# Performance work log

Hardware: AMD Instinct MI355X
Metric: run time of the kernel (lower is better)

The kernel has to match this reference:

```python
import jax, jax.numpy as jnp
import numpy as np

H = 8
DH = 64  # dim_head = dim // h
SCALE = DH ** -0.5
MEM_LEN = 512
CMEM_LEN = 128
RATIO = 4
SEQ_LEN = 512


def setup_inputs() -> dict:
    key = jax.random.key(0)
    ks = jax.random.split(key, 10)
    b, t, d = 8, 512, 512
    s = 0.02
    return {
        'x': jax.random.normal(ks[0], (b, t, d), jnp.float32),
        'mem': jax.random.normal(ks[1], (b, MEM_LEN, d), jnp.float32),
        'cmem': jax.random.normal(ks[2], (b, CMEM_LEN, d), jnp.float32),
        'Wq': jax.random.normal(ks[3], (d, d), jnp.float32) * s,
        'Wkv': jax.random.normal(ks[4], (2 * d, d), jnp.float32) * s,
        'Wo': jax.random.normal(ks[5], (d, d), jnp.float32) * s,
        'bo': jnp.zeros((d,), jnp.float32),
        'conv_w': jax.random.normal(ks[6], (d, d, RATIO), jnp.float32) * s,  # Conv1d OIH
        'conv_b': jnp.zeros((d,), jnp.float32),
        'deconv_w': jax.random.normal(ks[7], (MEM_LEN, CMEM_LEN), jnp.float32) * s,  # Linear(cmem_len, mem_len)
        'deconv_b': jnp.zeros((MEM_LEN,), jnp.float32),
    }


def _merge_heads(t):
    b, n, _ = t.shape
    return t.reshape(b, n, H, DH).transpose(0, 2, 1, 3)  # [b,h,n,dh]


def _full_attn(q, k, v):
    dots = jnp.einsum('bhid,bhjd->bhij', q, k) * (q.shape[-1] ** -0.5)
    return jnp.einsum('bhij,bhjd->bhid', jax.nn.softmax(dots, axis=-1), v)


def reference(x, mem, cmem, Wq, Wkv, Wo, bo, conv_w, conv_b, deconv_w, deconv_b):
    b, t, d = x.shape
    mem_len, cmem_len = mem.shape[1], cmem.shape[1]
    # projections
    q = x @ Wq.T
    kv_input = jnp.concatenate([cmem, mem, x], axis=1)  # [b, kv_len, d]
    kv = kv_input @ Wkv.T
    k, v = jnp.split(kv, 2, axis=-1)
    q, k, v = map(_merge_heads, (q, k, v))
    # main attention with causal mask offset by total memory length
    dots = jnp.einsum('bhid,bhjd->bhij', q, k) * SCALE  # [b,h,t,kv_len]
    total_mem = mem_len + cmem_len
    neg = -jnp.finfo(dots.dtype).max
    i = jnp.arange(t)[:, None]
    j = jnp.arange(t + total_mem)[None, :]
    causal = j > (i + total_mem)  # triu(diagonal=1+total_mem)
    dots = jnp.where(causal[None, None], neg, dots)
    attn = jax.nn.softmax(dots, axis=-1)
    out = jnp.einsum('bhij,bhjd->bhid', attn, v).transpose(0, 2, 1, 3).reshape(b, t, d)
    logits = out @ Wo.T + bo
    # FIFO memory update
    queue = jnp.concatenate([mem, x], axis=1)
    old_mem = jax.lax.stop_gradient(queue[:, :queue.shape[1] - MEM_LEN])  # evicted, detached
    new_mem = queue[:, -MEM_LEN:]
    # conv compression (old_mem length == SEQ_LEN, divisible by RATIO -> no pad)
    cm = jax.lax.conv_general_dilated(old_mem.transpose(0, 2, 1), conv_w, (RATIO,), 'VALID',
                                      dimension_numbers=('NCH', 'OIH', 'NCH'))
    compressed = (cm + conv_b[None, :, None]).transpose(0, 2, 1)  # [b, L/ratio, d]
    new_cmem = jnp.concatenate([cmem, compressed], axis=1)[:, -CMEM_LEN:]
    # reconstruction attention loss
    ckv = compressed @ Wkv.T
    cmem_k, cmem_v = map(_merge_heads, jnp.split(ckv, 2, axis=-1))
    kv_len = k.shape[2]
    lo = kv_len - min(mem_len, MEM_LEN) - SEQ_LEN
    hi = kv_len - SEQ_LEN
    qd = jax.lax.stop_gradient(q)
    omk = jax.lax.stop_gradient(k[:, :, lo:hi])
    omv = jax.lax.stop_gradient(v[:, :, lo:hi])
    aux_loss = jnp.mean((_full_attn(qd, omk, omv) - _full_attn(qd, cmem_k, cmem_v)) ** 2)
    # autoencoding loss via deconv Linear(cmem_len -> mem_len) over the seq axis
    recon = (new_cmem.transpose(0, 2, 1) @ deconv_w.T + deconv_b).transpose(0, 2, 1)  # [b, MEM_LEN, d]
    ae_loss = jnp.mean((old_mem - recon) ** 2)
    return (logits, new_mem, new_cmem, aux_loss, ae_loss)
```

## Files before the change

kernel.cpp:

```cpp
#include <hip/hip_runtime.h>

typedef __bf16 bf16x8 __attribute__((ext_vector_type(8)));
typedef float f32x4 __attribute__((ext_vector_type(4)));
typedef float f32x16 __attribute__((ext_vector_type(16)));
typedef unsigned short u16;
typedef unsigned int u32;

#define TLEN 512
#define DMODEL 512
#define DH 64
#define KVLEN 1152
#define TOTALMEM 640

__device__ inline u16 f2b(float f) {
    union { float f; u32 u; } x; x.f = f;
    u32 u = x.u;
    return (u16)((u + 0x7FFFu + ((u >> 16) & 1u)) >> 16);
}

__device__ inline float wave_red_sum(float v) {
#pragma unroll
    for (int off = 1; off < 64; off <<= 1) v += __shfl_xor(v, off);
    return v;
}

__device__ inline void gload16(const u16* g, u16* l) {
    __builtin_amdgcn_global_load_lds((const __attribute__((address_space(1))) void*)g,
                                     (__attribute__((address_space(3))) void*)l, 16, 0, 0);
}

__device__ __forceinline__ u32 cvtpk_bf16(float lo, float hi) {
    u32 r;
    asm("v_cvt_pk_bf16_f32 %0, %1, %2" : "=v"(r) : "v"(lo), "v"(hi));
    return r;
}

__global__ __launch_bounds__(256)
void prep_kernel(const float* __restrict__ x, const float* __restrict__ mem,
                 const float* __restrict__ cmem, const float* __restrict__ Wq,
                 const float* __restrict__ Wkv, const float* __restrict__ Wo,
                 const float* __restrict__ cw, const float* __restrict__ dw,
                 u16* __restrict__ kvin, u16* __restrict__ wq_b, u16* __restrict__ wkv_b,
                 u16* __restrict__ wo_b, u16* __restrict__ cw2, u16* __restrict__ dwb,
                 float* __restrict__ newmem, float* __restrict__ accs) {
    int idx = blockIdx.x * 256 + threadIdx.x;
    if (idx == 0) { accs[0] = 0.f; accs[1] = 0.f; accs[2] = 0.f; accs[3] = 0.f; }
    int e = idx * 4;
    float4 v;
    u16* o;
    if (e < 4718592) {
        int row = e >> 9, col = e & 511;
        int b = row / KVLEN, p = row - b * KVLEN;
        const float* src;
        if (p < 128)       src = cmem + ((size_t)(b * 128 + p)) * 512 + col;
        else if (p < 640)  src = mem  + ((size_t)(b * 512 + (p - 128))) * 512 + col;
        else               src = x    + ((size_t)(b * 512 + (p - 640))) * 512 + col;
        v = *(const float4*)src;
        o = kvin + e;
        if (p >= 640)
            *(float4*)(newmem + ((size_t)(b * 512 + (p - 640)) * 512 + col)) = v;
    } else if (e < 4980736) {
        int t = e - 4718592; v = *(const float4*)(Wq + t); o = wq_b + t;
    } else if (e < 5505024) {
        int t = e - 4980736; v = *(const float4*)(Wkv + t); o = wkv_b + t;
    } else if (e < 5767168) {
        int t = e - 5505024; v = *(const float4*)(Wo + t); o = wo_b + t;
    } else if (e < 6815744) {
        int t = e - 5767168;
        int oo = t >> 11, rem = t & 2047, tt = rem >> 9, ii = rem & 511;
        const float* s0 = cw + oo * 2048 + tt;
        v.x = s0[(ii + 0) * 4]; v.y = s0[(ii + 1) * 4];
        v.z = s0[(ii + 2) * 4]; v.w = s0[(ii + 3) * 4];
        o = cw2 + t;
    } else {
        int t = e - 6815744;
        v = *(const float4*)(dw + t); o = dwb + t;
    }
    o[0] = f2b(v.x); o[1] = f2b(v.y); o[2] = f2b(v.z); o[3] = f2b(v.w);
}

__device__ __forceinline__ void gemm_dev(
    const u16* __restrict__ A, int lda, int rowsPerB, long long bstride,
    const u16* __restrict__ Bt, int ldb, int Kb,
    float* __restrict__ Cpart, int partStride,
    float* __restrict__ Cf, u16* __restrict__ Cb, int ldc,
    const float* __restrict__ bias,
    int bx, int by, int bz, u16* As, u16* Bs) {
    const int tid = threadIdx.x;
    const int lane = tid & 63, wave = tid >> 6;
    const int wr = (wave >> 1) * 64, wc = (wave & 1) * 64;
    const int fr = lane & 15, fg = lane >> 4;
    const int arow0 = bx * 128;
    const int brow0 = by * 128;
    const int k0start = bz * Kb;

    const int lrow = lane >> 2;
    const int lcol = (lane & 3) * 8;
    const u16* gA[2]; const u16* gB[2];
#pragma unroll
    for (int i = 0; i < 2; ++i) {
        int r = wave * 32 + i * 16 + lrow;
        int gr = arow0 + r;
        int bb = gr / rowsPerB;
        int lr = gr - bb * rowsPerB;
        gA[i] = A + (size_t)bb * bstride + (size_t)lr * lda + k0start + lcol;
        gB[i] = Bt + (size_t)(brow0 + r) * ldb + k0start + lcol;
    }
    u16* lA0 = &As[(wave * 32) * 32];
    u16* lA1 = &As[(wave * 32 + 16) * 32];
    u16* lB0 = &Bs[(wave * 32) * 32];
    u16* lB1 = &Bs[(wave * 32 + 16) * 32];

    f32x4 acc[4][4] = {};
    for (int k = 0; k < Kb; k += 32) {
        __syncthreads();
        gload16(gA[0] + k, lA0);
        gload16(gA[1] + k, lA1);
        gload16(gB[0] + k, lB0);
        gload16(gB[1] + k, lB1);
        __syncthreads();
        bf16x8 af[4], bfr[4];
#pragma unroll
        for (int m = 0; m < 4; ++m) af[m] = *(bf16x8*)&As[(wr + m * 16 + fr) * 32 + fg * 8];
#pragma unroll
        for (int n = 0; n < 4; ++n) bfr[n] = *(bf16x8*)&Bs[(wc + n * 16 + fr) * 32 + fg * 8];
#pragma unroll
        for (int m = 0; m < 4; ++m)
#pragma unroll
            for (int n = 0; n < 4; ++n)
                acc[m][n] = __builtin_amdgcn_mfma_f32_16x16x32_bf16(af[m], bfr[n], acc[m][n], 0, 0, 0);
    }

#pragma unroll
    for (int m = 0; m < 4; ++m)
#pragma unroll
        for (int n = 0; n < 4; ++n)
#pragma unroll
            for (int r = 0; r < 4; ++r) {
                int row = arow0 + wr + m * 16 + fg * 4 + r;
                int col = brow0 + wc + n * 16 + fr;
                float v = acc[m][n][r];
                if (Cpart) {
                    Cpart[(size_t)bz * partStride + (size_t)row * ldc + col] = v;
                } else {
                    if (bias) v += bias[col];
                    if (Cf) Cf[(size_t)row * ldc + col] = v;
                    if (Cb) Cb[(size_t)row * ldc + col] = f2b(v);
                }
            }
}

__global__ __launch_bounds__(256)
void gemm3(const u16* __restrict__ kvin, const u16* __restrict__ wq,
           const u16* __restrict__ wkv, const u16* __restrict__ cw2,
           u16* __restrict__ q_bf, u16* __restrict__ kv_bf, float* __restrict__ part) {
    __shared__ u16 As[128 * 32];
    __shared__ u16 Bs[128 * 32];
    int id = blockIdx.x;
    if (id < 128) {
        gemm_dev(kvin + 327680, 512, 512, 589824, wq, 512, 512,
                 nullptr, 0, nullptr, q_bf, 512, nullptr,
                 id & 31, id >> 5, 0, As, Bs);
    } else if (id < 704) {
        int t = id - 128;
        gemm_dev(kvin, 512, 9216, 0, wkv, 512, 512,
                 nullptr, 0, nullptr, kv_bf, 1024, nullptr,
                 t % 72, t / 72, 0, As, Bs);
    } else {
        int t = id - 704;
        gemm_dev(kvin + 65536, 2048, 128, 589824, cw2, 2048, 512,
                 part, 524288, nullptr, nullptr, 512, nullptr,
                 t & 7, (t >> 3) & 3, t >> 5, As, Bs);
    }
}

__global__ __launch_bounds__(256)
void gemm_full(const u16* __restrict__ A, int lda, int rowsPerB, long long bstride,
               const u16* __restrict__ Bt, int ldb, int Kb,
               float* __restrict__ Cf, u16* __restrict__ Cb, int ldc,
               const float* __restrict__ bias) {
    __shared__ u16 As[128 * 32];
    __shared__ u16 Bs[128 * 32];
    gemm_dev(A, lda, rowsPerB, bstride, Bt, ldb, Kb, nullptr, 0, Cf, Cb, ldc,
             bias, blockIdx.x, blockIdx.y, 0, As, Bs);
}

__global__ __launch_bounds__(256)
void conv_reduce(const float* __restrict__ part, const float* __restrict__ cb,
                 float* __restrict__ outf, u16* __restrict__ outb) {
    int idx = (blockIdx.x * 256 + threadIdx.x) * 4;
    float4 s = *(const float4*)(part + idx);
#pragma unroll
    for (int sp = 1; sp < 4; ++sp) {
        float4 p = *(const float4*)(part + (size_t)sp * 524288 + idx);
        s.x += p.x; s.y += p.y; s.z += p.z; s.w += p.w;
    }
    float4 bb = *(const float4*)(cb + (idx & 511));
    s.x += bb.x; s.y += bb.y; s.z += bb.z; s.w += bb.w;
    *(float4*)(outf + idx) = s;
    outb[idx + 0] = f2b(s.x); outb[idx + 1] = f2b(s.y);
    outb[idx + 2] = f2b(s.z); outb[idx + 3] = f2b(s.w);
}

__device__ __forceinline__ void transpose_dev(const u16* __restrict__ kv,
                                              u16* __restrict__ vT, int rowsPerB,
                                              int jt, int bh, u16* t_s) {
    int b = bh >> 3, h = bh & 7;
    int tid = threadIdx.x;
    int jr = tid >> 2, c0 = (tid & 3) * 16;
    const u16* g = kv + (size_t)(b * rowsPerB + jt * 64 + jr) * 1024 + 512 + h * DH + c0;
#pragma unroll
    for (int u = 0; u < 16; ++u) t_s[jr * 65 + c0 + u] = g[u];
    __syncthreads();
    int dh = tid >> 2, j0 = (tid & 3) * 16;
    union { u16 us[8]; bf16x8 v8; } o1, o2;
#pragma unroll
    for (int u = 0; u < 8; ++u) {
        o1.us[u] = t_s[(j0 + u) * 65 + dh];
        o2.us[u] = t_s[(j0 + 8 + u) * 65 + dh];
    }
    u16* o = vT + (size_t)(bh * DH + dh) * rowsPerB + jt * 64 + j0;
    *(bf16x8*)o = o1.v8;
    *(bf16x8*)(o + 8) = o2.v8;
}

__global__ __launch_bounds__(256)
void transpose2(const u16* __restrict__ kv, u16* __restrict__ vTm_,
                const u16* __restrict__ ckv, u16* __restrict__ vTc_,
                const u16* __restrict__ comp, u16* __restrict__ compT) {
    __shared__ u16 t_s[64 * 65];
    int bx = blockIdx.x, bh = blockIdx.y;
    if (bx < 18) { transpose_dev(kv, vTm_, KVLEN, bx, bh, t_s); return; }
    if (bx < 20) { transpose_dev(ckv, vTc_, 128, bx - 18, bh, t_s); return; }
    int idq = (bx - 20) * 64 + bh;
    int b = idq >> 4, tile = idq & 15;
    int rt = tile >> 3, ct = tile & 7;
    int tid = threadIdx.x;
    int jr = tid >> 2, c0 = (tid & 3) * 16;
    const u16* g = comp + (size_t)(b * 128 + rt * 64 + jr) * 512 + ct * 64 + c0;
#pragma unroll
    for (int u = 0; u < 16; ++u) t_s[jr * 65 + c0 + u] = g[u];
    __syncthreads();
    int dh = tid >> 2, j0 = (tid & 3) * 16;
    union { u16 us[8]; bf16x8 v8; } o1, o2;
#pragma unroll
    for (int u = 0; u < 8; ++u) {
        o1.us[u] = t_s[(j0 + u) * 65 + dh];
        o2.us[u] = t_s[(j0 + 8 + u) * 65 + dh];
    }
    u16* o = compT + (size_t)(b * 512 + ct * 64 + dh) * 128 + rt * 64 + j0;
    *(bf16x8*)o = o1.v8;
    *(bf16x8*)(o + 8) = o2.v8;
}

template <bool MASK>
__device__ __forceinline__ void attn_pass(
    const u16* __restrict__ kbase, int kstride,
    const u16* __restrict__ vbase, int vstride,
    int njt, int tid, int iq_min,
    const bf16x8* qf, u16* k_s, u16* v_s,
    f32x16& o0, f32x16& o1, float& m_run, float& l_run)
{
    const int lane = tid & 63;
    const int c31 = lane & 31;
    const int hi = lane >> 5;
    const int hi4 = hi << 2;
    const int srow = tid >> 2, ssl = tid & 3;
    const int kwa = srow * 64 + ((ssl ^ (srow & 7)) << 3);
    const int kwb = srow * 64 + (((ssl + 4) ^ (srow & 7)) << 3);
    const int iq = iq_min + c31;

    int krd[2][4];
#pragma unroll
    for (int jsub = 0; jsub < 2; ++jsub) {
        int row = jsub * 32 + c31;
#pragma unroll
        for (int ks = 0; ks < 4; ++ks)
            krd[jsub][ks] = row * 64 + (((2 * ks + hi) ^ (row & 7)) << 3);
    }
    int vrd[2][4];
#pragma unroll
    for (int half = 0; half < 2; ++half) {
        int row = half * 32 + c31;
#pragma unroll
        for (int s = 0; s < 4; ++s)
            vrd[half][s] = row * 64 + (((2 * s + hi) ^ (row & 7)) << 3);
    }

    float4 lk0, lk1, lv0, lv1;
#define AT_LOAD(T) { \
        const u16* gk = kbase + (size_t)((T) * 64 + srow) * kstride + ssl * 8; \
        lk0 = *(const float4*)gk; lk1 = *(const float4*)(gk + 32); \
        const u16* gv = vbase + (size_t)srow * vstride + (T) * 64 + ssl * 8; \
        lv0 = *(const float4*)gv; lv1 = *(const float4*)(gv + 32); }
#define AT_STORE(B) { \
        u16* kd = k_s + (B) * 4096; u16* vd = v_s + (B) * 4096; \
        *(float4*)(kd + kwa) = lk0; *(float4*)(kd + kwb) = lk1; \
        *(float4*)(vd + kwa) = lv0; *(float4*)(vd + kwb) = lv1; }

    AT_LOAD(0); AT_STORE(0);
    __syncthreads();

    for (int t = 0; t < njt; ++t) {
        const int cur = t & 1;
        if (t + 1 < njt) AT_LOAD(t + 1);
        const u16* ks_ = k_s + cur * 4096;
        const u16* vs_ = v_s + cur * 4096;

        f32x16 sA = {}, sB = {};
#pragma unroll
        for (int ks = 0; ks < 4; ++ks) {
            bf16x8 a0 = *(const bf16x8*)&ks_[krd[0][ks]];
            sA = __builtin_amdgcn_mfma_f32_32x32x16_bf16(a0, qf[ks], sA, 0, 0, 0);
        }
#pragma unroll
        for (int ks = 0; ks < 4; ++ks) {
            bf16x8 a1 = *(const bf16x8*)&ks_[krd[1][ks]];
            sB = __builtin_amdgcn_mfma_f32_32x32x16_bf16(a1, qf[ks], sB, 0, 0, 0);
        }
        if (MASK) {
            if (t * 64 + 63 > iq_min + TOTALMEM) {
#pragma unroll
                for (int r = 0; r < 16; ++r) {
                    int rj = (r & 3) + 8 * (r >> 2) + hi4;
                    if (t * 64 + rj > iq + TOTALMEM) sA[r] = -1e30f;
                    if (t * 64 + 32 + rj > iq + TOTALMEM) sB[r] = -1e30f;
                }
            }
        }
        float tmax = sA[0];
#pragma unroll
        for (int r = 1; r < 16; ++r) tmax = fmaxf(tmax, sA[r]);
#pragma unroll
        for (int r = 0; r < 16; ++r) tmax = fmaxf(tmax, sB[r]);
        tmax = fmaxf(tmax, __shfl_xor(tmax, 32));
        tmax *= 0.125f;
        if (__any(tmax > m_run + 8.0f)) {
            float m_new = fmaxf(m_run, tmax);
            float scl = __expf(m_run - m_new);
            m_run = m_new;
            l_run *= scl;
#pragma unroll
            for (int r = 0; r < 16; ++r) {
                float sc = __shfl(scl, (r & 3) + 8 * (r >> 2) + hi4);
                o0[r] *= sc; o1[r] *= sc;
            }
        }
        const float negm = -m_run;
        float ps = 0.f;
#pragma unroll
        for (int jsub = 0; jsub < 2; ++jsub) {
#pragma unroll
            for (int ksub = 0; ksub < 2; ++ksub) {
                float p0 = __expf(fmaf((jsub ? sB[ksub * 8 + 0] : sA[ksub * 8 + 0]), 0.125f, negm));
                float p1 = __expf(fmaf((jsub ? sB[ksub * 8 + 1] : sA[ksub * 8 + 1]), 0.125f, negm));
                float p2 = __expf(fmaf((jsub ? sB[ksub * 8 + 2] : sA[ksub * 8 + 2]), 0.125f, negm));
                float p3 = __expf(fmaf((jsub ? sB[ksub * 8 + 3] : sA[ksub * 8 + 3]), 0.125f, negm));
                float p4 = __expf(fmaf((jsub ? sB[ksub * 8 + 4] : sA[ksub * 8 + 4]), 0.125f, negm));
                float p5 = __expf(fmaf((jsub ? sB[ksub * 8 + 5] : sA[ksub * 8 + 5]), 0.125f, negm));
                float p6 = __expf(fmaf((jsub ? sB[ksub * 8 + 6] : sA[ksub * 8 + 6]), 0.125f, negm));
                float p7 = __expf(fmaf((jsub ? sB[ksub * 8 + 7] : sA[ksub * 8 + 7]), 0.125f, negm));
                ps += ((p0 + p1) + (p2 + p3)) + ((p4 + p5) + (p6 + p7));
                u32 X = cvtpk_bf16(p0, p1);
                u32 Z = cvtpk_bf16(p2, p3);
                u32 Y = cvtpk_bf16(p4, p5);
                u32 W = cvtpk_bf16(p6, p7);
                auto s1 = __builtin_amdgcn_permlane32_swap(X, Y, false, false);
                auto s2 = __builtin_amdgcn_permlane32_swap(Z, W, false, false);
                union { u32 w[4]; bf16x8 v; } fa;
                fa.w[0] = (u32)s1[0]; fa.w[1] = (u32)s2[0];
                fa.w[2] = (u32)s1[1]; fa.w[3] = (u32)s2[1];
                bf16x8 bv0 = *(const bf16x8*)&vs_[vrd[0][jsub * 2 + ksub]];
                bf16x8 bv1 = *(const bf16x8*)&vs_[vrd[1][jsub * 2 + ksub]];
                o0 = __builtin_amdgcn_mfma_f32_32x32x16_bf16(fa.v, bv0, o0, 0, 0, 0);
                o1 = __builtin_amdgcn_mfma_f32_32x32x16_bf16(fa.v, bv1, o1, 0, 0, 0);
            }
        }
        ps += __shfl_xor(ps, 32);
        l_run += ps;
        if (t + 1 < njt) AT_STORE(cur ^ 1);
        __syncthreads();
    }
#undef AT_LOAD
#undef AT_STORE
}

__global__ __launch_bounds__(256)
void attn_fused(const u16* __restrict__ q_bf, const u16* __restrict__ kv,
                const u16* __restrict__ vTm_, const u16* __restrict__ ckv,
                const u16* __restrict__ vTc_, u16* __restrict__ out_bf,
                float* __restrict__ acc_sum) {
    __shared__ u16 k_s[2 * 4096];
    __shared__ u16 v_s[2 * 4096];
    __shared__ float red_s[4];
    const int id = blockIdx.x;
    const int tid = threadIdx.x;
    const int w = tid >> 6, lane = tid & 63;
    const int c31 = lane & 31, hi4 = (lane >> 5) << 2;

    if (id < 256) {
        const int it = id & 3, bh = id >> 2;
        const int b = bh >> 3, h = bh & 7;
        const int iwmin = it * 128 + w * 32;
        const int iq = iwmin + c31;

        bf16x8 qf[4];
#pragma unroll
        for (int ks = 0; ks < 4; ++ks)
            qf[ks] = *(const bf16x8*)&q_bf[(size_t)(b * TLEN + iq) * DMODEL + h * DH + ks * 16 + hi4 * 2];

        const u16* kbase = kv + (size_t)b * KVLEN * 1024 + h * DH;
        const u16* vbase = vTm_ + (size_t)(bh * DH) * KVLEN;
        const int njt = ((it * 128 + 767) >> 6) + 1;

        f32x16 o0 = {}, o1 = {};
        float m_run = -1e30f, l_run = 0.f;
        attn_pass<true>(kbase, 1024, vbase, KVLEN, njt, tid, iwmin, qf, k_s, v_s, o0, o1, m_run, l_run);

        float linv = 1.0f / l_run;
#pragma unroll
        for (int r = 0; r < 16; ++r) {
            int R = (r & 3) + 8 * (r >> 2) + hi4;
            float li = __shfl(linv, R);
            int i = iwmin + R;
            u16* o = out_bf + (size_t)(b * TLEN + i) * DMODEL + h * DH + c31;
            o[0]  = f2b(o0[r] * li);
            o[32] = f2b(o1[r] * li);
        }
    } else {
        const int t2 = id - 256;
        const int it = t2 & 3, bh = t2 >> 2;
        const int b = bh >> 3, h = bh & 7;
        const int iwmin = it * 128 + w * 32;
        const int iq = iwmin + c31;

        bf16x8 qf[4];
#pragma unroll
        for (int ks = 0; ks < 4; ++ks)
            qf[ks] = *(const bf16x8*)&q_bf[(size_t)(b * TLEN + iq) * DMODEL + h * DH + ks * 16 + hi4 * 2];

        f32x16 o0 = {}, o1 = {};
        float m_run = -1e30f, l_run = 0.f;
        attn_pass<false>(kv + (size_t)(b * KVLEN + 128) * 1024 + h * DH, 1024,
                         vTm_ + (size_t)(bh * DH) * KVLEN + 128, KVLEN, 8,
                         tid, 0, qf, k_s, v_s, o0, o1, m_run, l_run);
        float n0[16], n1[16];
        {
            float linv = 1.0f / l_run;
#pragma unroll
            for (int r = 0; r < 16; ++r) {
                float li = __shfl(linv, (r & 3) + 8 * (r >> 2) + hi4);
                n0[r] = o0[r] * li;
                n1[r] = o1[r] * li;
            }
        }
        f32x16 c0 = {}, c1 = {};
        m_run = -1e30f; l_run = 0.f;
        attn_pass<false>(ckv + (size_t)(b * 128) * 1024 + h * DH, 1024,
                         vTc_ + (size_t)(bh * DH) * 128, 128, 2,
                         tid, 0, qf, k_s, v_s, c0, c1, m_run, l_run);
        float lsum = 0.f;
        {
            float linv = 1.0f / l_run;
#pragma unroll
            for (int r = 0; r < 16; ++r) {
                float li = __shfl(linv, (r & 3) + 8 * (r >> 2) + hi4);
                float d0 = n0[r] - c0[r] * li;
                float d1 = n1[r] - c1[r] * li;
                lsum += d0 * d0 + d1 * d1;
            }
        }
        lsum = wave_red_sum(lsum);
        if (lane == 0) red_s[w] = lsum;
        __syncthreads();
        if (tid == 0) atomicAdd(acc_sum, red_s[0] + red_s[1] + red_s[2] + red_s[3]);
    }
}

__global__ __launch_bounds__(256)
void tail2(const u16* __restrict__ attn_bf, const u16* __restrict__ wo_b,
           const float* __restrict__ bo, float* __restrict__ logits,
           const u16* __restrict__ dwb, const u16* __restrict__ compT,
           const float* __restrict__ mem, const float* __restrict__ db,
           float* __restrict__ accs, float* __restrict__ scal_out) {
    __shared__ __align__(16) char smem[16400];
    const int id = blockIdx.x;
    const int tid = threadIdx.x;
    u16* As = (u16*)smem;
    u16* Bs = (u16*)(smem + 8192);

    if (id < 128) {
        gemm_dev(attn_bf, 512, 4096, 0, wo_b, 512, 512,
                 nullptr, 0, logits, nullptr, 512, bo, id & 31, id >> 5, 0, As, Bs);
        return;
    }
    float* red = (float*)(smem + 16384);
    const int t = id - 128;
    const int b = t >> 4;
    const int bx = (t >> 2) & 3, by = t & 3;
    const int lane = tid & 63, wave = tid >> 6;
    const int wr = (wave >> 1) * 64, wc = (wave & 1) * 64;
    const int fr = lane & 15, fg = lane >> 4;
    const int arow0 = bx * 128, brow0 = by * 128;
    const int lrow = lane >> 2, lcol = (lane & 3) * 8;
    const u16* gA[2]; const u16* gB[2];
#pragma unroll
    for (int i = 0; i < 2; ++i) {
        int r = wave * 32 + i * 16 + lrow;
        gA[i] = dwb + (size_t)(arow0 + r) * 128 + lcol;
        gB[i] = compT + (size_t)(b * 512 + brow0 + r) * 128 + lcol;
    }
    u16* lA0 = &As[(wave * 32) * 32];
    u16* lA1 = &As[(wave * 32 + 16) * 32];
    u16* lB0 = &Bs[(wave * 32) * 32];
    u16* lB1 = &Bs[(wave * 32 + 16) * 32];

    f32x4 acc[4][4] = {};
    for (int k = 0; k < 128; k += 32) {
        __syncthreads();
        gload16(gA[0] + k, lA0);
        gload16(gA[1] + k, lA1);
        gload16(gB[0] + k, lB0);
        gload16(gB[1] + k, lB1);
        __syncthreads();
        bf16x8 af[4], bfr[4];
#pragma unroll
        for (int m = 0; m < 4; ++m) af[m] = *(bf16x8*)&As[(wr + m * 16 + fr) * 32 + fg * 8];
#pragma unroll
        for (int n = 0; n < 4; ++n) bfr[n] = *(bf16x8*)&Bs[(wc + n * 16 + fr) * 32 + fg * 8];
#pragma unroll
        for (int m = 0; m < 4; ++m)
#pragma unroll
            for (int n = 0; n < 4; ++n)
                acc[m][n] = __builtin_amdgcn_mfma_f32_16x16x32_bf16(af[m], bfr[n], acc[m][n], 0, 0, 0);
    }

    float lsum = 0.f;
#pragma unroll
    for (int m = 0; m < 4; ++m)
#pragma unroll
        for (int n = 0; n < 4; ++n)
#pragma unroll
            for (int rr = 0; rr < 4; ++rr) {
                int row = arow0 + wr + m * 16 + fg * 4 + rr;
                int col = brow0 + wc + n * 16 + fr;
                float v = acc[m][n][rr] + db[row];
                float d = mem[(size_t)(b * 512 + row) * 512 + col] - v;
                lsum = fmaf(d, d, lsum);
            }
    lsum = wave_red_sum(lsum);
    if (lane == 0) red[wave] = lsum;
    __syncthreads();
    if (tid == 0) {
        atomicAdd(accs + 1, red[0] + red[1] + red[2] + red[3]);
        __threadfence();
        u32 c = atomicAdd((u32*)(accs + 2), 1u);
        if (c == 127u) {
            float a0 = atomicAdd(accs + 0, 0.f);
            float a1 = atomicAdd(accs + 1, 0.f);
            scal_out[0] = a0 * (1.f / 2097152.f);
            scal_out[1] = a1 * (1.f / 2097152.f);
        }
    }
}

extern "C" void kernel_launch(void* const* d_in, const int* in_sizes, int n_in,
                              void* d_out, int out_size, void* d_ws, size_t ws_size,
                              hipStream_t stream) {
    const float* x      = (const float*)d_in[0];
    const float* mem    = (const float*)d_in[1];
    const float* cmem   = (const float*)d_in[2];
    const float* Wq     = (const float*)d_in[3];
    const float* Wkv    = (const float*)d_in[4];
    const float* Wo     = (const float*)d_in[5];
    const float* bo     = (const float*)d_in[6];
    const float* conv_w = (const float*)d_in[7];
    const float* conv_b = (const float*)d_in[8];
    const float* deconv_w = (const float*)d_in[9];
    const float* deconv_b = (const float*)d_in[10];
    float* out = (float*)d_out;

    char* w = (char*)d_ws;
    auto alloc = [&](size_t bytes) { char* p = w; w += (bytes + 255) & ~255ull; return p; };
    u16* Wq_bf   = (u16*)alloc(262144 * 2);
    u16* Wkv_bf  = (u16*)alloc(524288 * 2);
    u16* Wo_bf   = (u16*)alloc(262144 * 2);
    u16* cw2_bf  = (u16*)alloc(1048576 * 2);
    u16* dwb_bf  = (u16*)alloc(65536 * 2);
    u16* kvin_bf = (u16*)alloc(4718592 * 2);
    u16* q_bf    = (u16*)alloc(2097152 * 2);
    u16* kv_bf   = (u16*)alloc(9437184 * 2);
    u16* comp_bf = (u16*)alloc(524288 * 2);
    u16* compT   = (u16*)alloc(524288 * 2);
    u16* ckv_bf  = (u16*)alloc(1048576 * 2);
    u16* vTm     = (u16*)alloc(4718592 * 2);
    u16* vTc     = (u16*)alloc(524288 * 2);
    u16* attn_bf = (u16*)alloc(2097152 * 2);
    float* part  = (float*)alloc(4 * 524288 * 4);
    float* accs  = (float*)alloc(256);

    float* logits_o  = out;
    float* newmem_o  = out + 2097152;
    float* newcmem_o = out + 4194304;
    float* scalars_o = out + 4718592;

    prep_kernel<<<6720, 256, 0, stream>>>(x, mem, cmem, Wq, Wkv, Wo, conv_w, deconv_w,
                                          kvin_bf, Wq_bf, Wkv_bf, Wo_bf, cw2_bf, dwb_bf,
                                          newmem_o, accs);

    gemm3<<<832, 256, 0, stream>>>(kvin_bf, Wq_bf, Wkv_bf, cw2_bf, q_bf, kv_bf, part);

    conv_reduce<<<512, 256, 0, stream>>>(part, conv_b, newcmem_o, comp_bf);

    gemm_full<<<dim3(8, 8), 256, 0, stream>>>(comp_bf, 512, 1024, 0, Wkv_bf, 512, 512,
                                              nullptr, ckv_bf, 1024, nullptr);

    transpose2<<<dim3(22, 64), 256, 0, stream>>>(kv_bf, vTm, ckv_bf, vTc, comp_bf, compT);

    attn_fused<<<512, 256, 0, stream>>>(q_bf, kv_bf, vTm, ckv_bf, vTc, attn_bf, accs);

    tail2<<<256, 256, 0, stream>>>(attn_bf, Wo_bf, bo, logits_o,
                                   dwb_bf, compT, mem, deconv_b,
                                   accs, scalars_o);
}
```

Before: 126.2 us.

## Drop split-K conv GEMM and regroup mid-stage kernels to cut launches

The conv compression GEMM now runs with its full K=2048 in 32 blocks that write bias-added fp32 and bf16 outputs directly, so the partial-sum buffer and the conv_reduce kernel are gone. These long-K blocks are scheduled first in gemm3 so they start early. The compressed-KV GEMM, the comp transpose and the V transpose are merged into one mid kernel, with a small separate kernel for the cmem V transpose. Launch count drops by one and the partial-sum round-trip is removed, at the cost of a long serial K loop on only 32 blocks, which may become the critical path.

```diff
diff --git a/kernel.cpp b/kernel.cpp
--- a/kernel.cpp
+++ b/kernel.cpp
@@ -82,17 +82,15 @@
 __device__ __forceinline__ void gemm_dev(
     const u16* __restrict__ A, int lda, int rowsPerB, long long bstride,
     const u16* __restrict__ Bt, int ldb, int Kb,
-    float* __restrict__ Cpart, int partStride,
     float* __restrict__ Cf, u16* __restrict__ Cb, int ldc,
     const float* __restrict__ bias,
-    int bx, int by, int bz, u16* As, u16* Bs) {
+    int bx, int by, u16* As, u16* Bs) {
     const int tid = threadIdx.x;
     const int lane = tid & 63, wave = tid >> 6;
     const int wr = (wave >> 1) * 64, wc = (wave & 1) * 64;
     const int fr = lane & 15, fg = lane >> 4;
     const int arow0 = bx * 128;
     const int brow0 = by * 128;
-    const int k0start = bz * Kb;
 
     const int lrow = lane >> 2;
     const int lcol = (lane & 3) * 8;
@@ -103,8 +101,8 @@
         int gr = arow0 + r;
         int bb = gr / rowsPerB;
         int lr = gr - bb * rowsPerB;
-        gA[i] = A + (size_t)bb * bstride + (size_t)lr * lda + k0start + lcol;
-        gB[i] = Bt + (size_t)(brow0 + r) * ldb + k0start + lcol;
+        gA[i] = A + (size_t)bb * bstride + (size_t)lr * lda + lcol;
+        gB[i] = Bt + (size_t)(brow0 + r) * ldb + lcol;
     }
     u16* lA0 = &As[(wave * 32) * 32];
     u16* lA1 = &As[(wave * 32 + 16) * 32];
@@ -140,66 +138,33 @@
                 int row = arow0 + wr + m * 16 + fg * 4 + r;
                 int col = brow0 + wc + n * 16 + fr;
                 float v = acc[m][n][r];
-                if (Cpart) {
-                    Cpart[(size_t)bz * partStride + (size_t)row * ldc + col] = v;
-                } else {
-                    if (bias) v += bias[col];
-                    if (Cf) Cf[(size_t)row * ldc + col] = v;
-                    if (Cb) Cb[(size_t)row * ldc + col] = f2b(v);
-                }
+                if (bias) v += bias[col];
+                if (Cf) Cf[(size_t)row * ldc + col] = v;
+                if (Cb) Cb[(size_t)row * ldc + col] = f2b(v);
             }
 }
 
 __global__ __launch_bounds__(256)
 void gemm3(const u16* __restrict__ kvin, const u16* __restrict__ wq,
            const u16* __restrict__ wkv, const u16* __restrict__ cw2,
-           u16* __restrict__ q_bf, u16* __restrict__ kv_bf, float* __restrict__ part) {
+           const float* __restrict__ conv_b,
+           u16* __restrict__ q_bf, u16* __restrict__ kv_bf,
+           float* __restrict__ newcmem, u16* __restrict__ comp_bf) {
     __shared__ u16 As[128 * 32];
     __shared__ u16 Bs[128 * 32];
     int id = blockIdx.x;
-    if (id < 128) {
+    if (id < 32) {
+        gemm_dev(kvin + 65536, 2048, 128, 589824, cw2, 2048, 2048,
+                 newcmem, comp_bf, 512, conv_b, id & 7, id >> 3, As, Bs);
+    } else if (id < 160) {
+        int t = id - 32;
         gemm_dev(kvin + 327680, 512, 512, 589824, wq, 512, 512,
-                 nullptr, 0, nullptr, q_bf, 512, nullptr,
-                 id & 31, id >> 5, 0, As, Bs);
-    } else if (id < 704) {
-        int t = id - 128;
+                 nullptr, q_bf, 512, nullptr, t & 31, t >> 5, As, Bs);
+    } else {
+        int t = id - 160;
         gemm_dev(kvin, 512, 9216, 0, wkv, 512, 512,
-                 nullptr, 0, nullptr, kv_bf, 1024, nullptr,
-                 t % 72, t / 72, 0, As, Bs);
-    } else {
-        int t = id - 704;
-        gemm_dev(kvin + 65536, 2048, 128, 589824, cw2, 2048, 512,
-                 part, 524288, nullptr, nullptr, 512, nullptr,
-                 t & 7, (t >> 3) & 3, t >> 5, As, Bs);
-    }
-}
-
-__global__ __launch_bounds__(256)
-void gemm_full(const u16* __restrict__ A, int lda, int rowsPerB, long long bstride,
-               const u16* __restrict__ Bt, int ldb, int Kb,
-               float* __restrict__ Cf, u16* __restrict__ Cb, int ldc,
-               const float* __restrict__ bias) {
-    __shared__ u16 As[128 * 32];
-    __shared__ u16 Bs[128 * 32];
-    gemm_dev(A, lda, rowsPerB, bstride, Bt, ldb, Kb, nullptr, 0, Cf, Cb, ldc,
-             bias, blockIdx.x, blockIdx.y, 0, As, Bs);
-}
-
-__global__ __launch_bounds__(256)
-void conv_reduce(const float* __restrict__ part, const float* __restrict__ cb,
-                 float* __restrict__ outf, u16* __restrict__ outb) {
-    int idx = (blockIdx.x * 256 + threadIdx.x) * 4;
-    float4 s = *(const float4*)(part + idx);
-#pragma unroll
-    for (int sp = 1; sp < 4; ++sp) {
-        float4 p = *(const float4*)(part + (size_t)sp * 524288 + idx);
-        s.x += p.x; s.y += p.y; s.z += p.z; s.w += p.w;
-    }
-    float4 bb = *(const float4*)(cb + (idx & 511));
-    s.x += bb.x; s.y += bb.y; s.z += bb.z; s.w += bb.w;
-    *(float4*)(outf + idx) = s;
-    outb[idx + 0] = f2b(s.x); outb[idx + 1] = f2b(s.y);
-    outb[idx + 2] = f2b(s.z); outb[idx + 3] = f2b(s.w);
+                 nullptr, kv_bf, 1024, nullptr, t % 72, t / 72, As, Bs);
+    }
 }
 
 __device__ __forceinline__ void transpose_dev(const u16* __restrict__ kv,
@@ -225,32 +190,49 @@
 }
 
 __global__ __launch_bounds__(256)
-void transpose2(const u16* __restrict__ kv, u16* __restrict__ vTm_,
-                const u16* __restrict__ ckv, u16* __restrict__ vTc_,
-                const u16* __restrict__ comp, u16* __restrict__ compT) {
+void mid_kernel(const u16* __restrict__ comp, const u16* __restrict__ wkv,
+                u16* __restrict__ ckv, u16* __restrict__ compT,
+                const u16* __restrict__ kv, u16* __restrict__ vTm_) {
+    __shared__ __align__(16) char smem[16640];
+    int id = blockIdx.x;
+    int tid = threadIdx.x;
+    if (id < 64) {
+        u16* As = (u16*)smem;
+        u16* Bs = (u16*)(smem + 8192);
+        gemm_dev(comp, 512, 1024, 0, wkv, 512, 512,
+                 nullptr, ckv, 1024, nullptr, id & 7, id >> 3, As, Bs);
+        return;
+    }
+    u16* t_s = (u16*)smem;
+    if (id < 192) {
+        int idq = id - 64;
+        int b = idq >> 4, tile = idq & 15;
+        int rt = tile >> 3, ct = tile & 7;
+        int jr = tid >> 2, c0 = (tid & 3) * 16;
+        const u16* g = comp + (size_t)(b * 128 + rt * 64 + jr) * 512 + ct * 64 + c0;
+#pragma unroll
+        for (int u = 0; u < 16; ++u) t_s[jr * 65 + c0 + u] = g[u];
+        __syncthreads();
+        int dh = tid >> 2, j0 = (tid & 3) * 16;
+        union { u16 us[8]; bf16x8 v8; } o1, o2;
+#pragma unroll
+        for (int u = 0; u < 8; ++u) {
+            o1.us[u] = t_s[(j0 + u) * 65 + dh];
+            o2.us[u] = t_s[(j0 + 8 + u) * 65 + dh];
+        }
+        u16* o = compT + (size_t)(b * 512 + ct * 64 + dh) * 128 + rt * 64 + j0;
+        *(bf16x8*)o = o1.v8;
+        *(bf16x8*)(o + 8) = o2.v8;
+        return;
+    }
+    int t = id - 192;
+    transpose_dev(kv, vTm_, KVLEN, t % 18, t / 18, t_s);
+}
+
+__global__ __launch_bounds__(256)
+void vtc_kernel(const u16* __restrict__ ckv, u16* __restrict__ vTc_) {
     __shared__ u16 t_s[64 * 65];
-    int bx = blockIdx.x, bh = blockIdx.y;
-    if (bx < 18) { transpose_dev(kv, vTm_, KVLEN, bx, bh, t_s); return; }
-    if (bx < 20) { transpose_dev(ckv, vTc_, 128, bx - 18, bh, t_s); return; }
-    int idq = (bx - 20) * 64 + bh;
-    int b = idq >> 4, tile = idq & 15;
-    int rt = tile >> 3, ct = tile & 7;
-    int tid = threadIdx.x;
-    int jr = tid >> 2, c0 = (tid & 3) * 16;
-    const u16* g = comp + (size_t)(b * 128 + rt * 64 + jr) * 512 + ct * 64 + c0;
-#pragma unroll
-    for (int u = 0; u < 16; ++u) t_s[jr * 65 + c0 + u] = g[u];
-    __syncthreads();
-    int dh = tid >> 2, j0 = (tid & 3) * 16;
-    union { u16 us[8]; bf16x8 v8; } o1, o2;
-#pragma unroll
-    for (int u = 0; u < 8; ++u) {
-        o1.us[u] = t_s[(j0 + u) * 65 + dh];
-        o2.us[u] = t_s[(j0 + 8 + u) * 65 + dh];
-    }
-    u16* o = compT + (size_t)(b * 512 + ct * 64 + dh) * 128 + rt * 64 + j0;
-    *(bf16x8*)o = o1.v8;
-    *(bf16x8*)(o + 8) = o2.v8;
+    transpose_dev(ckv, vTc_, 128, blockIdx.x & 1, blockIdx.x >> 1, t_s);
 }
 
 template <bool MASK>
@@ -491,7 +473,7 @@
 
     if (id < 128) {
         gemm_dev(attn_bf, 512, 4096, 0, wo_b, 512, 512,
-                 nullptr, 0, logits, nullptr, 512, bo, id & 31, id >> 5, 0, As, Bs);
+                 logits, nullptr, 512, bo, id & 31, id >> 5, As, Bs);
         return;
     }
     float* red = (float*)(smem + 16384);
@@ -596,7 +578,6 @@
     u16* vTm     = (u16*)alloc(4718592 * 2);
     u16* vTc     = (u16*)alloc(524288 * 2);
     u16* attn_bf = (u16*)alloc(2097152 * 2);
-    float* part  = (float*)alloc(4 * 524288 * 4);
     float* accs  = (float*)alloc(256);
 
     float* logits_o  = out;
@@ -608,14 +589,12 @@
                                           kvin_bf, Wq_bf, Wkv_bf, Wo_bf, cw2_bf, dwb_bf,
                                           newmem_o, accs);
 
-    gemm3<<<832, 256, 0, stream>>>(kvin_bf, Wq_bf, Wkv_bf, cw2_bf, q_bf, kv_bf, part);
-
-    conv_reduce<<<512, 256, 0, stream>>>(part, conv_b, newcmem_o, comp_bf);
-
-    gemm_full<<<dim3(8, 8), 256, 0, stream>>>(comp_bf, 512, 1024, 0, Wkv_bf, 512, 512,
-                                              nullptr, ckv_bf, 1024, nullptr);
-
-    transpose2<<<dim3(22, 64), 256, 0, stream>>>(kv_bf, vTm, ckv_bf, vTc, comp_bf, compT);
+    gemm3<<<736, 256, 0, stream>>>(kvin_bf, Wq_bf, Wkv_bf, cw2_bf, conv_b,
+                                   q_bf, kv_bf, newcmem_o, comp_bf);
+
+    mid_kernel<<<1344, 256, 0, stream>>>(comp_bf, Wkv_bf, ckv_bf, compT, kv_bf, vTm);
+
+    vtc_kernel<<<128, 256, 0, stream>>>(ckv_bf, vTc);
 
     attn_fused<<<512, 256, 0, stream>>>(q_bf, kv_bf, vTm, ckv_bf, vTc, attn_bf, accs);
 
```

New measurement: 141.5 us. +12.1%, slower.
